# Optimization experiments

Measured on AMD Instinct MI355X. Metric: run time of the kernel, lower is better.

## Reference

```python
import jax, jax.numpy as jnp
import numpy as np

N_NODES = 100000


def gcn_conv(x, W, b, src, dst, n):
    # PyG GCNConv: h = X @ W, add self-loops, symmetric normalization, scatter-add, + bias
    h = x @ W  # [N, out]
    loop = jnp.arange(n, dtype=src.dtype)
    src2 = jnp.concatenate([src, loop])
    dst2 = jnp.concatenate([dst, loop])
    ew = jnp.ones(src2.shape[0], dtype=h.dtype)
    deg = jax.ops.segment_sum(ew, dst2, num_segments=n)  # in-degree incl. self-loop
    dinv = jnp.where(deg > 0, jax.lax.rsqrt(deg), 0.0)
    norm = dinv[src2] * dinv[dst2]  # [E+N]
    msg = h[src2] * norm[:, None]  # gather + scale
    out = jax.ops.segment_sum(msg, dst2, num_segments=n)  # scatter-add
    return out + b


def setup_inputs() -> dict:
    key = jax.random.key(0)
    k1, k2, k3, k4, k5 = jax.random.split(key, 5)
    n, e = N_NODES, 3200000
    d_in, d_hid, d_out = 512, 16, 7
    x = jax.random.normal(k1, (n, d_in), dtype=jnp.float32)
    edge_index = jax.random.randint(k2, (2, e), 0, n, dtype=jnp.int64)
    W1 = jax.random.normal(k3, (d_in, d_hid), dtype=jnp.float32) / np.sqrt(d_in)
    b1 = jnp.zeros((d_hid,), dtype=jnp.float32)
    W2 = jax.random.normal(k4, (d_hid, d_out), dtype=jnp.float32) / np.sqrt(d_hid)
    b2 = jnp.zeros((d_out,), dtype=jnp.float32)
    return {"x": x, "edge_index": edge_index, "W1": W1, "b1": b1, "W2": W2, "b2": b2}


def reference(x, edge_index, W1, b1, W2, b2):
    n = x.shape[0]
    src, dst = edge_index[0], edge_index[1]
    h = jax.nn.relu(gcn_conv(x, W1, b1, src, dst, n))
    # dropout is identity in eval mode
    h = gcn_conv(h, W2, b2, src, dst, n)
    return jax.nn.log_softmax(h, axis=1)
```

## Files before the change

### kernel.cpp

```cpp
#include <hip/hip_runtime.h>
#include <math.h>

#define D_IN 512
#define F1   16
#define F2   7

#define BKT_SHIFT 8
#define PK_SHIFT  18
#define PK_MASK   ((1u << PK_SHIFT) - 1u)
#define A_CHUNK   8192
#define B_CAP     16384

__global__ __launch_bounds__(256) void binhist_kernel(const int* __restrict__ dst,
                                                      int* __restrict__ bucket_cnt,
                                                      int E, int NB) {
    __shared__ int lh[512];
    for (int i = threadIdx.x; i < 512; i += 256) lh[i] = 0;
    __syncthreads();
    int base = blockIdx.x * A_CHUNK;
#pragma unroll
    for (int i = 0; i < A_CHUNK / 256; ++i) {
        int t = base + i * 256 + threadIdx.x;
        if (t < E) {
            int d = __builtin_nontemporal_load(&dst[t]);
            atomicAdd(&lh[d >> BKT_SHIFT], 1);
        }
    }
    __syncthreads();
    for (int i = threadIdx.x; i < NB; i += 256) {
        int v = lh[i];
        if (v) atomicAdd(&bucket_cnt[i], v);
    }
}

__global__ __launch_bounds__(512) void bucketscan_kernel(const int* __restrict__ bucket_cnt,
                                                         int* __restrict__ bucket_base,
                                                         int* __restrict__ bucket_cursor,
                                                         int NB, int E) {
    __shared__ int sm[512];
    int tid = threadIdx.x;
    int v = (tid < NB) ? bucket_cnt[tid] : 0;
    sm[tid] = v;
    __syncthreads();
    for (int off = 1; off < 512; off <<= 1) {
        int t = (tid >= off) ? sm[tid - off] : 0;
        __syncthreads();
        sm[tid] += t;
        __syncthreads();
    }
    if (tid < NB) {
        int ex = sm[tid] - v;
        bucket_base[tid] = ex;
        bucket_cursor[tid] = ex;
    }
    if (tid == 0) bucket_base[NB] = E;
}

__global__ __launch_bounds__(256) void bin_kernel(const int* __restrict__ src,
                                                  const int* __restrict__ dst,
                                                  int* __restrict__ bucket_cursor,
                                                  unsigned int* __restrict__ binned,
                                                  int E, int NB) {
    __shared__ int lh[512];
    __shared__ int lbase[512];
    __shared__ int lcur[512];
    __shared__ int sdelta[512];
    __shared__ int sA[512], sB[512];
    __shared__ unsigned int rbuf[A_CHUNK];
    __shared__ int rdelta[A_CHUNK];
    int tid = threadIdx.x;
    for (int i = tid; i < 512; i += 256) lh[i] = 0;
    __syncthreads();

    int base = blockIdx.x * A_CHUNK;
    int dcache[A_CHUNK / 256];
    int scache[A_CHUNK / 256];
#pragma unroll
    for (int i = 0; i < A_CHUNK / 256; ++i) {
        int t = base + i * 256 + tid;
        int d = -1, s = 0;
        if (t < E) {
            d = __builtin_nontemporal_load(&dst[t]);
            s = __builtin_nontemporal_load(&src[t]);
            atomicAdd(&lh[d >> BKT_SHIFT], 1);
        }
        dcache[i] = d;
        scache[i] = s;
    }
    __syncthreads();

    for (int i = tid; i < 512; i += 256) sA[i] = lh[i];
    __syncthreads();
    int* psrc = sA; int* pdst = sB;
    for (int off = 1; off < 512; off <<= 1) {
        for (int i = tid; i < 512; i += 256)
            pdst[i] = psrc[i] + ((i >= off) ? psrc[i - off] : 0);
        __syncthreads();
        int* tmp = psrc; psrc = pdst; pdst = tmp;
    }
    for (int i = tid; i < 512; i += 256) {
        int ex = psrc[i] - lh[i];
        lbase[i] = ex;
        lcur[i] = ex;
    }
    __syncthreads();

    for (int b = tid; b < NB; b += 256) {
        int c = lh[b];
        int g = c ? atomicAdd(&bucket_cursor[b], c) : 0;
        sdelta[b] = g - lbase[b];
    }
    __syncthreads();

#pragma unroll
    for (int i = 0; i < A_CHUNK / 256; ++i) {
        int d = dcache[i];
        if (d >= 0) {
            int b = d >> BKT_SHIFT;
            int p = atomicAdd(&lcur[b], 1);
            rbuf[p] = (unsigned int)scache[i] | ((unsigned int)(d & 255) << PK_SHIFT);
            rdelta[p] = sdelta[b];
        }
    }
    __syncthreads();

    int total = min(A_CHUNK, E - base);
    for (int p = tid; p < total; p += 256)
        binned[rdelta[p] + p] = rbuf[p];
}

__global__ __launch_bounds__(256) void csr_kernel(const unsigned int* __restrict__ binned,
                                                  const int* __restrict__ bucket_base,
                                                  int* __restrict__ row_ptr,
                                                  int* __restrict__ row_end,
                                                  float* __restrict__ dinv,
                                                  int* __restrict__ adj, int n) {
    __shared__ int lh[256], lscan[256], lcur[256];
    __shared__ unsigned int rbuf[B_CAP];
    int b = blockIdx.x;
    int tid = threadIdx.x;
    int gbase = bucket_base[b];
    int gend  = bucket_base[b + 1];
    int m = gend - gbase;
    lh[tid] = 0;
    __syncthreads();
    for (int i = tid; i < m; i += 256) {
        unsigned int w = __builtin_nontemporal_load(&binned[gbase + i]);
        if (i < B_CAP) rbuf[i] = w;
        atomicAdd(&lh[w >> PK_SHIFT], 1);
    }
    __syncthreads();
    int v = lh[tid];
    lscan[tid] = v;
    __syncthreads();
    for (int off = 1; off < 256; off <<= 1) {
        int t = (tid >= off) ? lscan[tid - off] : 0;
        __syncthreads();
        lscan[tid] += t;
        __syncthreads();
    }
    int ex = lscan[tid] - v;
    int node = (b << BKT_SHIFT) + tid;
    if (node < n) {
        row_ptr[node] = gbase + ex;
        row_end[node] = gbase + ex + v;
        dinv[node] = rsqrtf((float)v + 1.0f);
    }
    lcur[tid] = ex;
    __syncthreads();
    for (int i = tid; i < m; i += 256) {
        unsigned int w = (i < B_CAP) ? rbuf[i] : binned[gbase + i];
        int d = (int)(w >> PK_SHIFT);
        int s = (int)(w & PK_MASK);
        int p = atomicAdd(&lcur[d], 1);
        adj[gbase + p] = s;
    }
}

__global__ __launch_bounds__(256) void mm1_kernel(const float* __restrict__ x,
                                                  const float* __restrict__ W1,
                                                  const float* __restrict__ dinv,
                                                  float* __restrict__ h1s,
                                                  int n, int T) {
    int t = blockIdx.x * blockDim.x + threadIdx.x;
    if (t >= T) return;

    int idx[4];
    bool valid[4];
    const float4* xp[4];
#pragma unroll
    for (int u = 0; u < 4; ++u) {
        int nd = t + u * T;
        valid[u] = nd < n;
        idx[u] = valid[u] ? nd : 0;
        xp[u] = (const float4*)(x + (size_t)idx[u] * D_IN);
    }

    float acc[4][F1];
#pragma unroll
    for (int u = 0; u < 4; ++u)
#pragma unroll
        for (int j = 0; j < F1; ++j) acc[u][j] = 0.0f;

    for (int c = 0; c < D_IN / 4; ++c) {
        float4 av[4];
#pragma unroll
        for (int u = 0; u < 4; ++u) av[u] = xp[u][c];

        const float4* wr = (const float4*)(W1 + (size_t)c * 4 * F1);
#pragma unroll
        for (int kk = 0; kk < 4; ++kk) {
            float4 w[4];
#pragma unroll
            for (int q = 0; q < 4; ++q) w[q] = wr[kk * 4 + q];
            const float* wf = (const float*)w;
#pragma unroll
            for (int u = 0; u < 4; ++u) {
                float xe = ((const float*)&av[u])[kk];
#pragma unroll
                for (int j = 0; j < F1; ++j) acc[u][j] += xe * wf[j];
            }
        }
    }

#pragma unroll
    for (int u = 0; u < 4; ++u) {
        if (!valid[u]) continue;
        float di = dinv[idx[u]];
        float4* outp = (float4*)(h1s + (size_t)idx[u] * F1);
#pragma unroll
        for (int q = 0; q < 4; ++q)
            outp[q] = make_float4(acc[u][4 * q + 0] * di, acc[u][4 * q + 1] * di,
                                  acc[u][4 * q + 2] * di, acc[u][4 * q + 3] * di);
    }
}

__global__ __launch_bounds__(256) void agg1_kernel(const int* __restrict__ row_ptr,
                                                   const int* __restrict__ row_end,
                                                   const int* __restrict__ adj,
                                                   const float* __restrict__ h,
                                                   const float* __restrict__ dinv,
                                                   const float* __restrict__ b1,
                                                   float* __restrict__ acc, int n) {
    int t = blockIdx.x * 256 + threadIdx.x;
    int node = t >> 4, j = t & 15;
    if (node >= n) return;
    int s = row_ptr[node], e = row_end[node];
    float a0 = 0.0f, a1 = 0.0f;
    int k = s;
    for (; k + 1 < e; k += 2) {
        int s0 = adj[k], s1 = adj[k + 1];
        a0 += h[(size_t)s0 * F1 + j];
        a1 += h[(size_t)s1 * F1 + j];
    }
    if (k < e) a0 += h[(size_t)adj[k] * F1 + j];
    float di = dinv[node];
    float v = di * (a0 + a1 + h[(size_t)node * F1 + j]) + b1[j];
    acc[(size_t)node * F1 + j] = v > 0.0f ? v : 0.0f;
}

__global__ __launch_bounds__(256) void mm2_kernel(const float* __restrict__ hin,
                                                  const float* __restrict__ W2,
                                                  const float* __restrict__ dinv,
                                                  float* __restrict__ h2s, int n) {
    int t = blockIdx.x * blockDim.x + threadIdx.x;
    if (t >= n) return;
    const float4* hr = (const float4*)(hin + (size_t)t * F1);
    float hv[F1];
#pragma unroll
    for (int q = 0; q < 4; ++q) {
        float4 v = hr[q];
        hv[4 * q + 0] = v.x; hv[4 * q + 1] = v.y;
        hv[4 * q + 2] = v.z; hv[4 * q + 3] = v.w;
    }
    float acc[F2];
#pragma unroll
    for (int j = 0; j < F2; ++j) acc[j] = 0.0f;
#pragma unroll
    for (int k = 0; k < F1; ++k) {
        float xv = hv[k];
#pragma unroll
        for (int j = 0; j < F2; ++j) acc[j] += xv * W2[k * F2 + j];
    }
    float di = dinv[t];
    float* outp = h2s + (size_t)t * 8;
#pragma unroll
    for (int j = 0; j < F2; ++j) outp[j] = acc[j] * di;
    outp[7] = 0.0f;
}

__global__ __launch_bounds__(256) void agg2_kernel(const int* __restrict__ row_ptr,
                                                   const int* __restrict__ row_end,
                                                   const int* __restrict__ adj,
                                                   const float* __restrict__ h,
                                                   const float* __restrict__ dinv,
                                                   const float* __restrict__ b2,
                                                   float* __restrict__ out, int n) {
    int t = blockIdx.x * 256 + threadIdx.x;
    int node = t >> 3, j = t & 7;
    if (node >= n) return;
    int s = row_ptr[node], e = row_end[node];
    float a0 = 0.0f, a1 = 0.0f;
    int k = s;
    for (; k + 1 < e; k += 2) {
        int s0 = adj[k], s1 = adj[k + 1];
        a0 += h[(size_t)s0 * 8 + j];
        a1 += h[(size_t)s1 * 8 + j];
    }
    if (k < e) a0 += h[(size_t)adj[k] * 8 + j];
    float di = dinv[node];
    float bj = j < F2 ? b2[j] : 0.0f;
    float v = di * (a0 + a1 + h[(size_t)node * 8 + j]) + bj;
    if (j >= F2) v = -INFINITY;
    float m = v;
#pragma unroll
    for (int w = 1; w < 8; w <<= 1) m = fmaxf(m, __shfl_xor(m, w, 8));
    float ex = (j < F2) ? expf(v - m) : 0.0f;
    float sum = ex;
#pragma unroll
    for (int w = 1; w < 8; w <<= 1) sum += __shfl_xor(sum, w, 8);
    float lse = m + logf(sum);
    if (j < F2) out[(size_t)node * F2 + j] = v - lse;
}

extern "C" void kernel_launch(void* const* d_in, const int* in_sizes, int n_in,
                              void* d_out, int out_size, void* d_ws, size_t ws_size,
                              hipStream_t stream) {
    const float* x  = (const float*)d_in[0];
    const int*   ei = (const int*)d_in[1];
    const float* W1 = (const float*)d_in[2];
    const float* b1 = (const float*)d_in[3];
    const float* W2 = (const float*)d_in[4];
    const float* b2 = (const float*)d_in[5];

    int n = in_sizes[0] / D_IN;
    int E = in_sizes[1] / 2;
    const int* src = ei;
    const int* dst = ei + E;
    int NB = (n + 255) >> BKT_SHIFT;

    char* ws = (char*)d_ws;
    size_t o = 0;
    int* bucket_cnt    = (int*)(ws + o); o += 512 * 4;
    int* bucket_base   = (int*)(ws + o); o += 516 * 4;
    int* bucket_cursor = (int*)(ws + o); o += 512 * 4;
    int*   row_ptr = (int*)(ws + o);   o += (size_t)n * 4;
    int*   row_end = (int*)(ws + o);   o += (size_t)n * 4;
    float* dinv    = (float*)(ws + o); o += (size_t)n * 4;
    int*   adj     = (int*)(ws + o);   o += (size_t)E * 4;
    size_t uni = (size_t)E > (size_t)n * 32 ? (size_t)E : (size_t)n * 32;
    unsigned int* binned = (unsigned int*)(ws + o);
    float* h1s  = (float*)(ws + o);
    float* acc1 = (float*)(ws + o) + (size_t)n * F1;
    o += uni * 4;
    float* h2s = h1s;
    float* out = (float*)d_out;

    const int B = 256;
    int GA = (E + A_CHUNK - 1) / A_CHUNK;
    int gN = (n + B - 1) / B;

    hipMemsetAsync(bucket_cnt, 0, 512 * sizeof(int), stream);

    binhist_kernel<<<GA, B, 0, stream>>>(dst, bucket_cnt, E, NB);
    bucketscan_kernel<<<1, 512, 0, stream>>>(bucket_cnt, bucket_base, bucket_cursor, NB, E);
    bin_kernel<<<GA, B, 0, stream>>>(src, dst, bucket_cursor, binned, E, NB);
    csr_kernel<<<NB, B, 0, stream>>>(binned, bucket_base, row_ptr, row_end, dinv, adj, n);

    int T = (n + 3) / 4;
    mm1_kernel<<<(T + B - 1) / B, B, 0, stream>>>(x, W1, dinv, h1s, n, T);

    agg1_kernel<<<((size_t)n * F1 + B - 1) / B, B, 0, stream>>>(row_ptr, row_end, adj, h1s, dinv, b1, acc1, n);

    mm2_kernel<<<gN, B, 0, stream>>>(acc1, W2, dinv, h2s, n);

    agg2_kernel<<<((size_t)n * 8 + B - 1) / B, B, 0, stream>>>(row_ptr, row_end, adj, h2s, dinv, b2, out, n);
}
```

Measured before the change: 587.3 us.

## Split mm1 K dimension across four waves with shared-memory reduction

```diff
diff --git a/kernel.cpp b/kernel.cpp
--- a/kernel.cpp
+++ b/kernel.cpp
@@ -10,6 +10,7 @@
 #define PK_MASK   ((1u << PK_SHIFT) - 1u)
 #define A_CHUNK   8192
 #define B_CAP     16384
+#define NT        64
 
 __global__ __launch_bounds__(256) void binhist_kernel(const int* __restrict__ dst,
                                                       int* __restrict__ bucket_cnt,
@@ -180,58 +181,52 @@
 __global__ __launch_bounds__(256) void mm1_kernel(const float* __restrict__ x,
                                                   const float* __restrict__ W1,
                                                   const float* __restrict__ dinv,
-                                                  float* __restrict__ h1s,
-                                                  int n, int T) {
-    int t = blockIdx.x * blockDim.x + threadIdx.x;
-    if (t >= T) return;
-
-    int idx[4];
-    bool valid[4];
-    const float4* xp[4];
-#pragma unroll
-    for (int u = 0; u < 4; ++u) {
-        int nd = t + u * T;
-        valid[u] = nd < n;
-        idx[u] = valid[u] ? nd : 0;
-        xp[u] = (const float4*)(x + (size_t)idx[u] * D_IN);
-    }
-
-    float acc[4][F1];
-#pragma unroll
-    for (int u = 0; u < 4; ++u)
-#pragma unroll
-        for (int j = 0; j < F1; ++j) acc[u][j] = 0.0f;
-
-    for (int c = 0; c < D_IN / 4; ++c) {
-        float4 av[4];
-#pragma unroll
-        for (int u = 0; u < 4; ++u) av[u] = xp[u][c];
-
-        const float4* wr = (const float4*)(W1 + (size_t)c * 4 * F1);
+                                                  float* __restrict__ h1s, int n) {
+    __shared__ float red[4][NT][F1];
+    int tid = threadIdx.x;
+    int w = tid >> 6;
+    int l = tid & 63;
+    int node = blockIdx.x * NT + l;
+    int nd = node < n ? node : 0;
+
+    const float4* xp = (const float4*)(x + (size_t)nd * D_IN + (size_t)w * 128);
+    float acc[F1];
+#pragma unroll
+    for (int j = 0; j < F1; ++j) acc[j] = 0.0f;
+
+    for (int c = 0; c < 32; ++c) {
+        float4 xv = xp[c];
+        const float4* wr = (const float4*)(W1 + (size_t)(w * 128 + c * 4) * F1);
 #pragma unroll
         for (int kk = 0; kk < 4; ++kk) {
-            float4 w[4];
-#pragma unroll
-            for (int q = 0; q < 4; ++q) w[q] = wr[kk * 4 + q];
-            const float* wf = (const float*)w;
-#pragma unroll
-            for (int u = 0; u < 4; ++u) {
-                float xe = ((const float*)&av[u])[kk];
-#pragma unroll
-                for (int j = 0; j < F1; ++j) acc[u][j] += xe * wf[j];
-            }
-        }
-    }
-
-#pragma unroll
-    for (int u = 0; u < 4; ++u) {
-        if (!valid[u]) continue;
-        float di = dinv[idx[u]];
-        float4* outp = (float4*)(h1s + (size_t)idx[u] * F1);
-#pragma unroll
-        for (int q = 0; q < 4; ++q)
-            outp[q] = make_float4(acc[u][4 * q + 0] * di, acc[u][4 * q + 1] * di,
-                                  acc[u][4 * q + 2] * di, acc[u][4 * q + 3] * di);
+            float xe = ((const float*)&xv)[kk];
+            float4 w0 = wr[kk * 4 + 0], w1 = wr[kk * 4 + 1];
+            float4 w2 = wr[kk * 4 + 2], w3 = wr[kk * 4 + 3];
+            acc[ 0] += xe * w0.x; acc[ 1] += xe * w0.y; acc[ 2] += xe * w0.z; acc[ 3] += xe * w0.w;
+            acc[ 4] += xe * w1.x; acc[ 5] += xe * w1.y; acc[ 6] += xe * w1.z; acc[ 7] += xe * w1.w;
+            acc[ 8] += xe * w2.x; acc[ 9] += xe * w2.y; acc[10] += xe * w2.z; acc[11] += xe * w2.w;
+            acc[12] += xe * w3.x; acc[13] += xe * w3.y; acc[14] += xe * w3.z; acc[15] += xe * w3.w;
+        }
+    }
+
+#pragma unroll
+    for (int q = 0; q < 4; ++q)
+        ((float4*)&red[w][l][0])[q] = make_float4(acc[4 * q + 0], acc[4 * q + 1],
+                                                  acc[4 * q + 2], acc[4 * q + 3]);
+    __syncthreads();
+
+    int nl = tid >> 2, jg = (tid & 3) * 4;
+    int onode = blockIdx.x * NT + nl;
+    if (onode < n) {
+        float4 s = make_float4(0.f, 0.f, 0.f, 0.f);
+#pragma unroll
+        for (int ww = 0; ww < 4; ++ww) {
+            float4 p = *((const float4*)&red[ww][nl][jg]);
+            s.x += p.x; s.y += p.y; s.z += p.z; s.w += p.w;
+        }
+        float di = dinv[onode];
+        s.x *= di; s.y *= di; s.z *= di; s.w *= di;
+        *((float4*)(h1s + (size_t)onode * F1 + jg)) = s;
     }
 }
 
@@ -367,8 +362,7 @@
     bin_kernel<<<GA, B, 0, stream>>>(src, dst, bucket_cursor, binned, E, NB);
     csr_kernel<<<NB, B, 0, stream>>>(binned, bucket_base, row_ptr, row_end, dinv, adj, n);
 
-    int T = (n + 3) / 4;
-    mm1_kernel<<<(T + B - 1) / B, B, 0, stream>>>(x, W1, dinv, h1s, n, T);
+    mm1_kernel<<<(n + NT - 1) / NT, B, 0, stream>>>(x, W1, dinv, h1s, n);
 
     agg1_kernel<<<((size_t)n * F1 + B - 1) / B, B, 0, stream>>>(row_ptr, row_end, adj, h1s, dinv, b1, acc1, n);
 
```

Measured after the change: 579.9 us. No clear change (-1.3%).

## Rewrite X@W1 as wave-per-node with W1 in registers and shuffle reduction

Applied to the files above, without the earlier changes.

```diff
diff --git a/kernel.cpp b/kernel.cpp
--- a/kernel.cpp
+++ b/kernel.cpp
@@ -177,61 +177,74 @@
     }
 }
 
-__global__ __launch_bounds__(256) void mm1_kernel(const float* __restrict__ x,
-                                                  const float* __restrict__ W1,
-                                                  const float* __restrict__ dinv,
-                                                  float* __restrict__ h1s,
-                                                  int n, int T) {
-    int t = blockIdx.x * blockDim.x + threadIdx.x;
-    if (t >= T) return;
-
-    int idx[4];
-    bool valid[4];
-    const float4* xp[4];
-#pragma unroll
-    for (int u = 0; u < 4; ++u) {
-        int nd = t + u * T;
-        valid[u] = nd < n;
-        idx[u] = valid[u] ? nd : 0;
-        xp[u] = (const float4*)(x + (size_t)idx[u] * D_IN);
-    }
-
-    float acc[4][F1];
-#pragma unroll
-    for (int u = 0; u < 4; ++u)
-#pragma unroll
-        for (int j = 0; j < F1; ++j) acc[u][j] = 0.0f;
-
-    for (int c = 0; c < D_IN / 4; ++c) {
-        float4 av[4];
-#pragma unroll
-        for (int u = 0; u < 4; ++u) av[u] = xp[u][c];
-
-        const float4* wr = (const float4*)(W1 + (size_t)c * 4 * F1);
-#pragma unroll
-        for (int kk = 0; kk < 4; ++kk) {
-            float4 w[4];
-#pragma unroll
-            for (int q = 0; q < 4; ++q) w[q] = wr[kk * 4 + q];
-            const float* wf = (const float*)w;
-#pragma unroll
-            for (int u = 0; u < 4; ++u) {
-                float xe = ((const float*)&av[u])[kk];
-#pragma unroll
-                for (int j = 0; j < F1; ++j) acc[u][j] += xe * wf[j];
+__global__ __launch_bounds__(256, 2) void mm1_kernel(const float* __restrict__ x,
+                                                     const float* __restrict__ W1,
+                                                     const float* __restrict__ dinv,
+                                                     float* __restrict__ h1s, int n) {
+    int lane = threadIdx.x & 63;
+    int wave = (blockIdx.x * 256 + threadIdx.x) >> 6;
+    int NW = gridDim.x << 2;
+
+    float4 wreg[8][4];
+#pragma unroll
+    for (int g = 0; g < 2; ++g)
+#pragma unroll
+        for (int kl = 0; kl < 4; ++kl) {
+            const float4* wr = (const float4*)(W1 + (size_t)(g * 256 + 4 * lane + kl) * F1);
+#pragma unroll
+            for (int j4 = 0; j4 < 4; ++j4) wreg[g * 4 + kl][j4] = wr[j4];
+        }
+
+    int node = wave;
+    if (node >= n) return;
+    const float4* xr = (const float4*)(x + (size_t)node * D_IN);
+    float4 x0 = xr[lane], x1 = xr[64 + lane];
+
+    while (node < n) {
+        int nxt = node + NW;
+        float4 c0 = x0, c1 = x1;
+        if (nxt < n) {
+            const float4* xn = (const float4*)(x + (size_t)nxt * D_IN);
+            x0 = xn[lane]; x1 = xn[64 + lane];
+        }
+
+        float acc[F1];
+#pragma unroll
+        for (int j = 0; j < F1; ++j) acc[j] = 0.0f;
+#pragma unroll
+        for (int g = 0; g < 2; ++g) {
+            const float* xv = g == 0 ? (const float*)&c0 : (const float*)&c1;
+#pragma unroll
+            for (int kl = 0; kl < 4; ++kl) {
+                float xe = xv[kl];
+                const float* wf = (const float*)&wreg[g * 4 + kl][0];
+#pragma unroll
+                for (int j = 0; j < F1; ++j) acc[j] += xe * wf[j];
             }
         }
-    }
-
-#pragma unroll
-    for (int u = 0; u < 4; ++u) {
-        if (!valid[u]) continue;
-        float di = dinv[idx[u]];
-        float4* outp = (float4*)(h1s + (size_t)idx[u] * F1);
-#pragma unroll
-        for (int q = 0; q < 4; ++q)
-            outp[q] = make_float4(acc[u][4 * q + 0] * di, acc[u][4 * q + 1] * di,
-                                  acc[u][4 * q + 2] * di, acc[u][4 * q + 3] * di);
+
+        int c = F1;
+#pragma unroll
+        for (int m = 32; m >= 4; m >>= 1) {
+            int c2 = c >> 1;
+            bool hi = (lane & m) != 0;
+#pragma unroll
+            for (int i = 0; i < 8; ++i) {
+                if (i >= c2) break;
+                float send = hi ? acc[i] : acc[i + c2];
+                float keep = hi ? acc[i + c2] : acc[i];
+                acc[i] = keep + __shfl_xor(send, m);
+            }
+            c = c2;
+        }
+        acc[0] += __shfl_xor(acc[0], 1);
+        acc[0] += __shfl_xor(acc[0], 2);
+
+        float di = dinv[node];
+        if ((lane & 3) == 0)
+            h1s[(size_t)node * F1 + (lane >> 2)] = acc[0] * di;
+
+        node = nxt;
     }
 }
 
@@ -367,8 +380,7 @@
     bin_kernel<<<GA, B, 0, stream>>>(src, dst, bucket_cursor, binned, E, NB);
     csr_kernel<<<NB, B, 0, stream>>>(binned, bucket_base, row_ptr, row_end, dinv, adj, n);
 
-    int T = (n + 3) / 4;
-    mm1_kernel<<<(T + B - 1) / B, B, 0, stream>>>(x, W1, dinv, h1s, n, T);
+    mm1_kernel<<<512, B, 0, stream>>>(x, W1, dinv, h1s, n);
 
     agg1_kernel<<<((size_t)n * F1 + B - 1) / B, B, 0, stream>>>(row_ptr, row_end, adj, h1s, dinv, b1, acc1, n);
 
```

Measured after the change: 630.2 us. 1.07x slower.
